# Optimization experiments

Hardware: AMD Instinct MI355X
Metric: run time of the kernel (lower is better)

## Reference

```python
import jax, jax.numpy as jnp
import numpy as np

L = 16384   # sequence length
H = 1024    # feature dim
P = 1024    # state dim (ssm_size=2048, conj_sym=True -> P = ssm_size//2)
STEP_RESCALE = 1.0
CLIP_MAX = -1e-4


def setup_inputs() -> dict:
    key = jax.random.key(0)
    ks = jax.random.split(key, 7)
    log_dt_min, log_dt_max = np.log(0.001), np.log(0.1)
    return {
        "input_sequence": jax.random.normal(ks[0], (L, H), jnp.float32),
        # stable eigenvalues: negative real part
        "Lambda_re": -(jnp.abs(jax.random.normal(ks[1], (P,), jnp.float32)) + 1e-3),
        "Lambda_im": jax.random.normal(ks[2], (P,), jnp.float32) * jnp.pi,
        "B": jax.random.normal(ks[3], (P, H, 2), jnp.float32) / np.sqrt(H),
        "C": jax.random.normal(ks[4], (H, P, 2), jnp.float32) / np.sqrt(P),
        "D": jax.random.normal(ks[5], (H,), jnp.float32),
        "log_step": jax.random.uniform(ks[6], (P, 1), jnp.float32,
                                        minval=log_dt_min, maxval=log_dt_max),
    }


def _binop(q_i, q_j):
    # binary operator of the linear recurrence (diagonal A)
    A_i, b_i = q_i
    A_j, b_j = q_j
    return (A_j * A_i, A_j * b_i + b_j)


def reference(input_sequence, Lambda_re, Lambda_im, B, C, D, log_step):
    # clip_eigs=True: clamp real part at -1e-4
    Lambda = jnp.minimum(Lambda_re, CLIP_MAX) + 1j * Lambda_im        # (P,) complex64
    B_tilde = B[..., 0] + 1j * B[..., 1]                              # (P, H)
    C_tilde = C[..., 0] + 1j * C[..., 1]                              # (H, P)
    step = STEP_RESCALE * jnp.exp(log_step[:, 0])                     # (P,)
    # ZOH discretisation
    Lambda_bar = jnp.exp(Lambda * step)                               # (P,)
    B_bar = ((Lambda_bar - 1.0) / Lambda)[:, None] * B_tilde          # (P, H)
    # input projection: (L,H) @ (H,P) -> (L,P) complex
    Bu = input_sequence.astype(B_bar.dtype) @ B_bar.T
    Lam = jnp.broadcast_to(Lambda_bar, Bu.shape)                      # (L, P)
    # parallel (Blelchley-style) associative scan over time
    _, xs = jax.lax.associative_scan(_binop, (Lam, Bu))               # (L, P)
    # output projection; conj_sym=True -> factor 2 on the real part
    ys = 2.0 * jnp.real(xs @ C_tilde.T)                               # (L, H)
    return ys + input_sequence * D
```

## Files before the change

kernel.cpp:

```cpp
#include <hip/hip_runtime.h>
#include <hip/hip_bf16.h>
#include <stdint.h>


#define L_SEQ 16384
#define H_DIM 1024
#define P_DIM 1024
#define NCH   256
#define TCH   64

typedef __bf16 bf16x8 __attribute__((ext_vector_type(8)));
typedef float  floatx4 __attribute__((ext_vector_type(4)));
using bf16 = __hip_bfloat16;

__device__ __forceinline__ void gld_lds16(const void* g, void* l) {
    __builtin_amdgcn_global_load_lds(
        (const __attribute__((address_space(1))) uint32_t*)g,
        (__attribute__((address_space(3))) uint32_t*)l, 16, 0, 0);
}

__device__ __forceinline__ float lo_bf(uint32_t v) { return __uint_as_float(v << 16); }
__device__ __forceinline__ float hi_bf(uint32_t v) { return __uint_as_float(v & 0xffff0000u); }
__device__ __forceinline__ uint32_t pack_bf(float r, float i) {
    bf16 rb = __float2bfloat16(r), ib = __float2bfloat16(i);
    return ((uint32_t)(*(uint16_t*)&ib) << 16) | (uint32_t)(*(uint16_t*)&rb);
}

__device__ __forceinline__ float rd(const void* p, size_t i, int f) {
    return f ? ((const float*)p)[i]
             : __bfloat162float(((const bf16*)p)[i]);
}

__device__ __forceinline__ int detect_f32(const uint16_t* u) {
    __shared__ int cnt;
    if (threadIdx.x == 0) cnt = 0;
    __syncthreads();
    int c = 0;
    #pragma unroll
    for (int i = 0; i < 8; ++i) {
        int e = (u[threadIdx.x * 8 + i] >> 7) & 0xFF;
        c += (e >= 134);
    }
    if (c) atomicAdd(&cnt, c);
    __syncthreads();
    return cnt > 32;
}

__global__ void convert_u(const void* __restrict__ uin, bf16* __restrict__ ub) {
    const int f = detect_f32((const uint16_t*)uin);
    const size_t g = (size_t)blockIdx.x * 256 + threadIdx.x;
    if (f) {
        const float4* s = (const float4*)uin + g * 2;
        float4 a = s[0], b = s[1];
        alignas(16) bf16 t[8] = {
            __float2bfloat16(a.x), __float2bfloat16(a.y),
            __float2bfloat16(a.z), __float2bfloat16(a.w),
            __float2bfloat16(b.x), __float2bfloat16(b.y),
            __float2bfloat16(b.z), __float2bfloat16(b.w)};
        ((uint4*)ub)[g] = *(const uint4*)t;
    } else {
        ((uint4*)ub)[g] = ((const uint4*)uin)[g];
    }
}

__global__ void prep_all(const void* __restrict__ u,
                         const void* __restrict__ Lre, const void* __restrict__ Lim,
                         const void* __restrict__ lstep, const void* __restrict__ B,
                         const void* __restrict__ C, const void* __restrict__ D,
                         bf16* __restrict__ W1t, bf16* __restrict__ W2t,
                         float* __restrict__ d_f,
                         float2* __restrict__ lam, float2* __restrict__ lamT) {
    const int f = detect_f32((const uint16_t*)u);
    const int p = blockIdx.x;
    float lr = fminf(rd(Lre, p, f), -1e-4f);
    float li = rd(Lim, p, f);
    float s  = expf(rd(lstep, p, f));
    float ea = expf(lr * s);
    float lbr = ea * cosf(li * s), lbi = ea * sinf(li * s);
    float dr = lbr - 1.0f, di = lbi;
    float den = lr * lr + li * li;
    float cr = (dr * lr + di * li) / den;
    float ci = (di * lr - dr * li) / den;
    if (threadIdx.x == 0) {
        lam[p] = make_float2(lbr, lbi);
        float tr = lbr, ti = lbi;
        #pragma unroll
        for (int q = 0; q < 6; ++q) {
            float nr = tr * tr - ti * ti, ni = 2.0f * tr * ti;
            tr = nr; ti = ni;
        }
        lamT[p] = make_float2(tr, ti);
        d_f[p] = rd(D, p, f);
    }
    for (int h = threadIdx.x; h < H_DIM; h += blockDim.x) {
        size_t base = ((size_t)p * H_DIM + h) * 2;
        float br = rd(B, base + 0, f);
        float bi = rd(B, base + 1, f);
        W1t[(size_t)(2 * p)     * H_DIM + h] = __float2bfloat16(cr * br - ci * bi);
        W1t[(size_t)(2 * p + 1) * H_DIM + h] = __float2bfloat16(cr * bi + ci * br);
    }
    const int h = blockIdx.x;
    for (int q = threadIdx.x; q < P_DIM; q += blockDim.x) {
        size_t base = ((size_t)h * P_DIM + q) * 2;
        W2t[(size_t)h * (2 * P_DIM) + 2 * q]     = __float2bfloat16( 2.0f * rd(C, base + 0, f));
        W2t[(size_t)h * (2 * P_DIM) + 2 * q + 1] = __float2bfloat16(-2.0f * rd(C, base + 1, f));
    }
}

template <int N, int K, int MODE>
__global__ __launch_bounds__(256) void gemm_bt(
    const bf16* __restrict__ A, const bf16* __restrict__ Bt,
    bf16* __restrict__ OutBF, float* __restrict__ OutF,
    const bf16* __restrict__ U, const float* __restrict__ Dvec,
    const float2* __restrict__ lam, float2* __restrict__ aggp) {
    constexpr int NXB = N / 128;
    __shared__ alignas(16) uint8_t sA[128 * 128];
    __shared__ alignas(16) uint8_t sB[128 * 128];

    const int tid  = threadIdx.x;
    const int wave = tid >> 6;
    const int lane = tid & 63;
    const int bid = blockIdx.x;
    const int xr  = bid & 7;
    const int jj  = bid >> 3;
    const int bx  = jj % NXB;
    const int by  = (jj / NXB) * 8 + xr;
    const int bm  = by * 128, bn = bx * 128;
    const int wm  = (wave >> 1) * 64, wn = (wave & 1) * 64;

    floatx4 acc[4][4] = {};

    const int fr   = lane & 15;
    const int kq   = lane >> 4;
    const int srow = tid >> 3;
    const int skc  = tid & 7;

    for (int k0 = 0; k0 < K; k0 += 64) {
        #pragma unroll
        for (int q = 0; q < 4; ++q) {
            const int row = q * 32 + srow;
            const int kcg = skc ^ (row & 7);
            gld_lds16(A  + (size_t)(bm + row) * K + k0 + kcg * 8,
                      sA + q * 4096 + wave * 1024);
            gld_lds16(Bt + (size_t)(bn + row) * K + k0 + kcg * 8,
                      sB + q * 4096 + wave * 1024);
        }
        __syncthreads();
        #pragma unroll
        for (int s = 0; s < 2; ++s) {
            bf16x8 af[4], bfr[4];
            #pragma unroll
            for (int mi = 0; mi < 4; ++mi) {
                const int row = wm + mi * 16 + fr;
                const int ch  = (s * 4 + kq) ^ (row & 7);
                af[mi] = *(const bf16x8*)(sA + row * 128 + ch * 16);
            }
            #pragma unroll
            for (int ni = 0; ni < 4; ++ni) {
                const int row = wn + ni * 16 + fr;
                const int ch  = (s * 4 + kq) ^ (row & 7);
                bfr[ni] = *(const bf16x8*)(sB + row * 128 + ch * 16);
            }
            #pragma unroll
            for (int mi = 0; mi < 4; ++mi)
                #pragma unroll
                for (int ni = 0; ni < 4; ++ni)
                    acc[mi][ni] = __builtin_amdgcn_mfma_f32_16x16x32_bf16(
                        af[mi], bfr[ni], acc[mi][ni], 0, 0, 0);
        }
        __syncthreads();
    }

    const int col0  = bn + wn + fr;
    const int rbase = bm + wm + kq * 4;
    #pragma unroll
    for (int mi = 0; mi < 4; ++mi) {
        #pragma unroll
        for (int rr = 0; rr < 4; ++rr) {
            const int row = rbase + mi * 16 + rr;
            #pragma unroll
            for (int ni = 0; ni < 4; ++ni) {
                const int c = col0 + ni * 16;
                float v = acc[mi][ni][rr];
                if (MODE == 2) {
                    float uu = __bfloat162float(U[(size_t)row * H_DIM + c]);
                    __builtin_nontemporal_store(v + uu * Dvec[c],
                                                &OutF[(size_t)row * N + c]);
                } else {
                    OutBF[(size_t)row * N + c] = __float2bfloat16(v);
                }
            }
        }
    }

    if (MODE == 1) {
        const int par = fr & 1;
        const int cg  = (bm + wm) >> 6;
        #pragma unroll
        for (int ni = 0; ni < 4; ++ni) {
            const int ql = (wn + ni * 16 + (fr & ~1)) >> 1;
            const float2 lb = lam[(bn >> 1) + ql];
            const float l1r = lb.x, l1i = lb.y;
            const float l2r = l1r * l1r - l1i * l1i, l2i = 2.f * l1r * l1i;
            const float l4r = l2r * l2r - l2i * l2i, l4i = 2.f * l2r * l2i;
            const float l8r = l4r * l4r - l4i * l4i, l8i = 2.f * l4r * l4i;
            const float l12r = l8r * l4r - l8i * l4i;
            const float l12i = l8r * l4i + l8i * l4r;
            float wr_, wi_;
            if      (kq == 0) { wr_ = l12r; wi_ = l12i; }
            else if (kq == 1) { wr_ = l8r;  wi_ = l8i;  }
            else if (kq == 2) { wr_ = l4r;  wi_ = l4i;  }
            else              { wr_ = 1.f;  wi_ = 0.f;  }
            float s = 0.f;
            #pragma unroll
            for (int mi = 3; mi >= 0; --mi) {
                #pragma unroll
                for (int rr = 3; rr >= 0; --rr) {
                    float own  = acc[mi][ni][rr];
                    float part = __shfl_xor(own, 1);
                    s += wr_ * own + (par ? wi_ : -wi_) * part;
                    float nr = wr_ * l1r - wi_ * l1i;
                    float nI = wr_ * l1i + wi_ * l1r;
                    wr_ = nr; wi_ = nI;
                }
                float nr = wr_ * l12r - wi_ * l12i;
                float nI = wr_ * l12i + wi_ * l12r;
                wr_ = nr; wi_ = nI;
            }
            s += __shfl_xor(s, 16);
            s += __shfl_xor(s, 32);
            float other = __shfl_xor(s, 1);
            if (kq == 0 && par == 0)
                aggp[(size_t)cg * P_DIM + (bn >> 1) + ql] = make_float2(s, other);
        }
    }
}

__global__ void scan_phase2p(const float2* __restrict__ agg,
                             const float2* __restrict__ lamT,
                             float2* __restrict__ carry) {
    const int w = threadIdx.x >> 6;
    const int j = threadIdx.x & 63;
    const int p = blockIdx.x * 4 + w;
    const float2 A = lamT[p];
    float b2r = A.x * A.x - A.y * A.y, b2i = 2.f * A.x * A.y;
    float Br = b2r * b2r - b2i * b2i, Bi = 2.f * b2r * b2i;
    float2 a[4];
    #pragma unroll
    for (int k = 0; k < 4; ++k) a[k] = agg[(size_t)(4 * j + k) * P_DIM + p];
    float xr = 0.f, xi = 0.f;
    #pragma unroll
    for (int k = 0; k < 4; ++k) {
        float nr = A.x * xr - A.y * xi + a[k].x;
        float ni = A.x * xi + A.y * xr + a[k].y;
        xr = nr; xi = ni;
    }
    float cr = Br, ci = Bi, vr = xr, vi = xi;
    #pragma unroll
    for (int d = 1; d < 64; d <<= 1) {
        float pvr = __shfl_up(vr, d), pvi = __shfl_up(vi, d);
        float pcr = __shfl_up(cr, d), pci = __shfl_up(ci, d);
        if (j >= d) {
            float nvr = cr * pvr - ci * pvi + vr;
            float nvi = cr * pvi + ci * pvr + vi;
            float ncr = cr * pcr - ci * pci;
            float nci = cr * pci + ci * pcr;
            vr = nvr; vi = nvi; cr = ncr; ci = nci;
        }
    }
    float sr = __shfl_up(vr, 1), si = __shfl_up(vi, 1);
    if (j == 0) { sr = 0.f; si = 0.f; }
    #pragma unroll
    for (int k = 0; k < 4; ++k) {
        carry[(size_t)(4 * j + k) * P_DIM + p] = make_float2(sr, si);
        float nr = A.x * sr - A.y * si + a[k].x;
        float ni = A.x * si + A.y * sr + a[k].y;
        sr = nr; si = ni;
    }
}

__global__ void scan_phase3(uint32_t* __restrict__ BuX,
                            const float2* __restrict__ lam,
                            const float2* __restrict__ carry) {
    const int p = blockIdx.y * 256 + threadIdx.x;
    const int c = blockIdx.x;
    const float2 lb = lam[p];
    const float2 c0 = carry[(size_t)c * P_DIM + p];
    float xr = c0.x, xi = c0.y;
    uint32_t* b = BuX + (size_t)c * TCH * P_DIM + p;
    #pragma unroll 4
    for (int j = 0; j < TCH; ++j) {
        uint32_t v = *b;
        float nr = lb.x * xr - lb.y * xi + lo_bf(v);
        float ni = lb.x * xi + lb.y * xr + hi_bf(v);
        xr = nr; xi = ni;
        *b = pack_bf(xr, xi);
        b += P_DIM;
    }
}

extern "C" void kernel_launch(void* const* d_in, const int* in_sizes, int n_in,
                              void* d_out, int out_size, void* d_ws, size_t ws_size,
                              hipStream_t stream) {
    float* out = (float*)d_out;

    char* w = (char*)d_ws;
    w += 256;
    float2* lam   = (float2*)w;  w += (size_t)P_DIM * 8;
    float2* lamT  = (float2*)w;  w += (size_t)P_DIM * 8;
    float*  d_f   = (float*)w;   w += (size_t)H_DIM * 4;
    float2* agg   = (float2*)w;  w += (size_t)NCH * P_DIM * 8;
    float2* carry = (float2*)w;  w += (size_t)NCH * P_DIM * 8;
    bf16*   W1t   = (bf16*)w;    w += (size_t)2 * P_DIM * H_DIM * 2;
    bf16*   W2t   = (bf16*)w;    w += (size_t)H_DIM * 2 * P_DIM * 2;
    bf16*   ub    = (bf16*)w;    w += (size_t)L_SEQ * H_DIM * 2;
    bf16*   Xbuf  = (bf16*)w;

    convert_u<<<(L_SEQ * H_DIM / 8) / 256, 256, 0, stream>>>(d_in[0], ub);
    prep_all<<<P_DIM, 256, 0, stream>>>(d_in[0], d_in[1], d_in[2], d_in[6],
                                        d_in[3], d_in[4], d_in[5],
                                        W1t, W2t, d_f, lam, lamT);

    gemm_bt<2 * P_DIM, H_DIM, 1><<<(2 * P_DIM / 128) * 128, 256, 0, stream>>>(
        ub, W1t, Xbuf, nullptr, nullptr, nullptr, lam, agg);

    scan_phase2p<<<P_DIM / 4, 256, 0, stream>>>(agg, lamT, carry);
    scan_phase3<<<dim3(NCH, P_DIM / 256), 256, 0, stream>>>(
        (uint32_t*)Xbuf, lam, carry);

    gemm_bt<H_DIM, 2 * P_DIM, 2><<<(H_DIM / 128) * 128, 256, 0, stream>>>(
        Xbuf, W2t, nullptr, out, ub, d_f, nullptr, nullptr);
}
```

Before: 351.0 us.

## Use 256x256 double-buffered GEMM tiles with 8 waves and interleaved LDS/MFMA schedule

Replaces the 128x128 single-buffered GEMM with a 256x256 tile kernel run by 512 threads. It double-buffers K-tiles in LDS through async global-to-LDS loads, prefetching two tiles ahead, and interleaves LDS fragment reads with MFMA quarters under explicit barriers and priority hints. The larger tile raises arithmetic intensity and the pipelining hides load latency. The cost is 128KB of LDS per block and high register pressure from a 32-accumulator tile, which limits occupancy. The chunk-aggregate epilogue is adjusted so each wave now covers two 64-row chunks.

After: 332.8 us. 5.2% less time.

```diff
diff --git a/kernel.cpp b/kernel.cpp
--- a/kernel.cpp
+++ b/kernel.cpp
@@ -107,74 +107,123 @@
     }
 }
 
+
+#define STAGE(b, t) do {                                                      \
+    const int k0_ = (t) * 64;                                                 \
+    _Pragma("unroll")                                                         \
+    for (int q_ = 0; q_ < 4; ++q_) {                                          \
+        const int row_ = q_ * 64 + srow;                                      \
+        const int g_   = sg ^ (row_ & 7);                                     \
+        gld_lds16(A  + (size_t)(bm + row_) * K + k0_ + g_ * 8,                \
+                  sA + (b) * 32768 + q_ * 8192 + wave * 1024);                \
+        gld_lds16(Bt + (size_t)(bn + row_) * K + k0_ + g_ * 8,                \
+                  sB + (b) * 32768 + q_ * 8192 + wave * 1024);                \
+    } } while (0)
+
+#define LDA(b, mh) do {                                                       \
+    _Pragma("unroll")                                                         \
+    for (int mi_ = 0; mi_ < 4; ++mi_) {                                       \
+        const int row_ = wm + ((mh) * 4 + mi_) * 16 + fr;                     \
+        _Pragma("unroll")                                                     \
+        for (int ks_ = 0; ks_ < 2; ++ks_) {                                   \
+            const int ch_ = (ks_ * 4 + kq) ^ (row_ & 7);                      \
+            af[mi_][ks_] = *(const bf16x8*)(sA + (b) * 32768 + row_ * 128 + ch_ * 16); \
+        } } } while (0)
+
+#define LDB(b, nh) do {                                                       \
+    _Pragma("unroll")                                                         \
+    for (int ni_ = 0; ni_ < 2; ++ni_) {                                       \
+        const int row_ = wn + ((nh) * 2 + ni_) * 16 + fr;                     \
+        _Pragma("unroll")                                                     \
+        for (int ks_ = 0; ks_ < 2; ++ks_) {                                   \
+            const int ch_ = (ks_ * 4 + kq) ^ (row_ & 7);                      \
+            bfr[ni_][ks_] = *(const bf16x8*)(sB + (b) * 32768 + row_ * 128 + ch_ * 16); \
+        } } } while (0)
+
+#define MMA(mh, nh) do {                                                      \
+    asm volatile("s_waitcnt lgkmcnt(0)" ::: "memory");                        \
+    __builtin_amdgcn_sched_barrier(0);                                        \
+    __builtin_amdgcn_s_setprio(1);                                            \
+    _Pragma("unroll")                                                         \
+    for (int mi_ = 0; mi_ < 4; ++mi_)                                         \
+        _Pragma("unroll")                                                     \
+        for (int ni_ = 0; ni_ < 2; ++ni_)                                     \
+            _Pragma("unroll")                                                 \
+            for (int ks_ = 0; ks_ < 2; ++ks_)                                 \
+                acc[(mh) * 4 + mi_][(nh) * 2 + ni_] =                         \
+                    __builtin_amdgcn_mfma_f32_16x16x32_bf16(                  \
+                        af[mi_][ks_], bfr[ni_][ks_],                          \
+                        acc[(mh) * 4 + mi_][(nh) * 2 + ni_], 0, 0, 0);        \
+    __builtin_amdgcn_s_setprio(0);                                            \
+} while (0)
+
 template <int N, int K, int MODE>
-__global__ __launch_bounds__(256) void gemm_bt(
+__global__ __launch_bounds__(512, 2) void gemm256(
     const bf16* __restrict__ A, const bf16* __restrict__ Bt,
     bf16* __restrict__ OutBF, float* __restrict__ OutF,
     const bf16* __restrict__ U, const float* __restrict__ Dvec,
     const float2* __restrict__ lam, float2* __restrict__ aggp) {
-    constexpr int NXB = N / 128;
-    __shared__ alignas(16) uint8_t sA[128 * 128];
-    __shared__ alignas(16) uint8_t sB[128 * 128];
+    constexpr int NXB = N / 256;
+    constexpr int KT  = K / 64;
+    __shared__ alignas(16) uint8_t sA[2 * 32768];
+    __shared__ alignas(16) uint8_t sB[2 * 32768];
 
     const int tid  = threadIdx.x;
     const int wave = tid >> 6;
     const int lane = tid & 63;
-    const int bid = blockIdx.x;
-    const int xr  = bid & 7;
-    const int jj  = bid >> 3;
-    const int bx  = jj % NXB;
-    const int by  = (jj / NXB) * 8 + xr;
-    const int bm  = by * 128, bn = bx * 128;
-    const int wm  = (wave >> 1) * 64, wn = (wave & 1) * 64;
-
-    floatx4 acc[4][4] = {};
+    const int bid  = blockIdx.x;
+    const int xr   = bid & 7;
+    const int jj   = bid >> 3;
+    const int bx   = jj % NXB;
+    const int by   = (jj / NXB) * 8 + xr;
+    const int bm   = by * 256, bn = bx * 256;
+    const int wm   = (wave >> 2) * 128, wn = (wave & 3) * 64;
+
+    floatx4 acc[8][4] = {};
 
     const int fr   = lane & 15;
     const int kq   = lane >> 4;
     const int srow = tid >> 3;
-    const int skc  = tid & 7;
-
-    for (int k0 = 0; k0 < K; k0 += 64) {
-        #pragma unroll
-        for (int q = 0; q < 4; ++q) {
-            const int row = q * 32 + srow;
-            const int kcg = skc ^ (row & 7);
-            gld_lds16(A  + (size_t)(bm + row) * K + k0 + kcg * 8,
-                      sA + q * 4096 + wave * 1024);
-            gld_lds16(Bt + (size_t)(bn + row) * K + k0 + kcg * 8,
-                      sB + q * 4096 + wave * 1024);
-        }
-        __syncthreads();
-        #pragma unroll
-        for (int s = 0; s < 2; ++s) {
-            bf16x8 af[4], bfr[4];
-            #pragma unroll
-            for (int mi = 0; mi < 4; ++mi) {
-                const int row = wm + mi * 16 + fr;
-                const int ch  = (s * 4 + kq) ^ (row & 7);
-                af[mi] = *(const bf16x8*)(sA + row * 128 + ch * 16);
-            }
-            #pragma unroll
-            for (int ni = 0; ni < 4; ++ni) {
-                const int row = wn + ni * 16 + fr;
-                const int ch  = (s * 4 + kq) ^ (row & 7);
-                bfr[ni] = *(const bf16x8*)(sB + row * 128 + ch * 16);
-            }
-            #pragma unroll
-            for (int mi = 0; mi < 4; ++mi)
-                #pragma unroll
-                for (int ni = 0; ni < 4; ++ni)
-                    acc[mi][ni] = __builtin_amdgcn_mfma_f32_16x16x32_bf16(
-                        af[mi], bfr[ni], acc[mi][ni], 0, 0, 0);
-        }
-        __syncthreads();
+    const int sg   = tid & 7;
+
+    STAGE(0, 0);
+    STAGE(1, 1);
+    asm volatile("s_waitcnt vmcnt(8)" ::: "memory");
+    __builtin_amdgcn_sched_barrier(0);
+    __builtin_amdgcn_s_barrier();
+
+    bf16x8 af[4][2], bfr[2][2];
+
+    #pragma unroll 2
+    for (int t = 0; t < KT; ++t) {
+        const int cur = t & 1;
+        LDA(cur, 0); LDB(cur, 0);
+        __builtin_amdgcn_s_barrier();
+        MMA(0, 0);
+        LDB(cur, 1);
+        __builtin_amdgcn_s_barrier();
+        MMA(0, 1);
+        LDA(cur, 1);
+        __builtin_amdgcn_s_barrier();
+        MMA(1, 1);
+        LDB(cur, 0);
+        __builtin_amdgcn_s_barrier();
+        MMA(1, 0);
+        __builtin_amdgcn_s_barrier();
+        if (t + 2 < KT) {
+            STAGE(cur, t + 2);
+            asm volatile("s_waitcnt vmcnt(8)" ::: "memory");
+        } else {
+            asm volatile("s_waitcnt vmcnt(0)" ::: "memory");
+        }
+        __builtin_amdgcn_sched_barrier(0);
+        __builtin_amdgcn_s_barrier();
     }
 
     const int col0  = bn + wn + fr;
     const int rbase = bm + wm + kq * 4;
     #pragma unroll
-    for (int mi = 0; mi < 4; ++mi) {
+    for (int mi = 0; mi < 8; ++mi) {
         #pragma unroll
         for (int rr = 0; rr < 4; ++rr) {
             const int row = rbase + mi * 16 + rr;
@@ -195,7 +244,7 @@
 
     if (MODE == 1) {
         const int par = fr & 1;
-        const int cg  = (bm + wm) >> 6;
+        const int cg0 = (bm + wm) >> 6;
         #pragma unroll
         for (int ni = 0; ni < 4; ++ni) {
             const int ql = (wn + ni * 16 + (fr & ~1)) >> 1;
@@ -206,32 +255,36 @@
             const float l8r = l4r * l4r - l4i * l4i, l8i = 2.f * l4r * l4i;
             const float l12r = l8r * l4r - l8i * l4i;
             const float l12i = l8r * l4i + l8i * l4r;
-            float wr_, wi_;
-            if      (kq == 0) { wr_ = l12r; wi_ = l12i; }
-            else if (kq == 1) { wr_ = l8r;  wi_ = l8i;  }
-            else if (kq == 2) { wr_ = l4r;  wi_ = l4i;  }
-            else              { wr_ = 1.f;  wi_ = 0.f;  }
-            float s = 0.f;
             #pragma unroll
-            for (int mi = 3; mi >= 0; --mi) {
+            for (int h = 0; h < 2; ++h) {
+                float wr_, wi_;
+                if      (kq == 0) { wr_ = l12r; wi_ = l12i; }
+                else if (kq == 1) { wr_ = l8r;  wi_ = l8i;  }
+                else if (kq == 2) { wr_ = l4r;  wi_ = l4i;  }
+                else              { wr_ = 1.f;  wi_ = 0.f;  }
+                float s = 0.f;
                 #pragma unroll
-                for (int rr = 3; rr >= 0; --rr) {
-                    float own  = acc[mi][ni][rr];
-                    float part = __shfl_xor(own, 1);
-                    s += wr_ * own + (par ? wi_ : -wi_) * part;
-                    float nr = wr_ * l1r - wi_ * l1i;
-                    float nI = wr_ * l1i + wi_ * l1r;
+                for (int mi2 = 3; mi2 >= 0; --mi2) {
+                    #pragma unroll
+                    for (int rr = 3; rr >= 0; --rr) {
+                        float own  = acc[h * 4 + mi2][ni][rr];
+                        float part = __shfl_xor(own, 1);
+                        s += wr_ * own + (par ? wi_ : -wi_) * part;
+                        float nr = wr_ * l1r - wi_ * l1i;
+                        float nI = wr_ * l1i + wi_ * l1r;
+                        wr_ = nr; wi_ = nI;
+                    }
+                    float nr = wr_ * l12r - wi_ * l12i;
+                    float nI = wr_ * l12i + wi_ * l12r;
                     wr_ = nr; wi_ = nI;
                 }
-                float nr = wr_ * l12r - wi_ * l12i;
-                float nI = wr_ * l12i + wi_ * l12r;
-                wr_ = nr; wi_ = nI;
+                s += __shfl_xor(s, 16);
+                s += __shfl_xor(s, 32);
+                float other = __shfl_xor(s, 1);
+                if (kq == 0 && par == 0)
+                    aggp[(size_t)(cg0 + h) * P_DIM + (bn >> 1) + ql] =
+                        make_float2(s, other);
             }
-            s += __shfl_xor(s, 16);
-            s += __shfl_xor(s, 32);
-            float other = __shfl_xor(s, 1);
-            if (kq == 0 && par == 0)
-                aggp[(size_t)cg * P_DIM + (bn >> 1) + ql] = make_float2(s, other);
         }
     }
 }
@@ -321,13 +374,13 @@
                                         d_in[3], d_in[4], d_in[5],
                                         W1t, W2t, d_f, lam, lamT);
 
-    gemm_bt<2 * P_DIM, H_DIM, 1><<<(2 * P_DIM / 128) * 128, 256, 0, stream>>>(
+    gemm256<2 * P_DIM, H_DIM, 1><<<(2 * P_DIM / 256) * (L_SEQ / 256), 512, 0, stream>>>(
         ub, W1t, Xbuf, nullptr, nullptr, nullptr, lam, agg);
 
     scan_phase2p<<<P_DIM / 4, 256, 0, stream>>>(agg, lamT, carry);
     scan_phase3<<<dim3(NCH, P_DIM / 256), 256, 0, stream>>>(
         (uint32_t*)Xbuf, lam, carry);
 
-    gemm_bt<H_DIM, 2 * P_DIM, 2><<<(H_DIM / 128) * 128, 256, 0, stream>>>(
+    gemm256<H_DIM, 2 * P_DIM, 2><<<(H_DIM / 256) * (L_SEQ / 256), 512, 0, stream>>>(
         Xbuf, W2t, nullptr, out, ub, d_f, nullptr, nullptr);
 }
```
